# Kernel tuning notes

Measured on AMD Instinct MI355X. Metric: run time of the kernel, lower is better.

The kernel has to match this reference:

```python
import jax, jax.numpy as jnp
import numpy as np

NEG_SLOPE = 0.2  # PyG GATv2Conv default negative_slope


def gatv2_layer(x, src, dst, edge_attr, Wl, bl, Wr, br, We, att, bias, n_nodes):
    """Faithful PyG GATv2Conv (concat=True, eval mode / no dropout).
    x: [N, Fin]; src/dst: [E]; edge_attr: [E, Fe]; att: [H, C].
    Returns [N, H*C].
    """
    H, C = att.shape
    xl = (x @ Wl + bl).reshape(-1, H, C)        # source-side transform (x_j)
    xr = (x @ Wr + br).reshape(-1, H, C)        # target-side transform (x_i)
    e_emb = (edge_attr @ We).reshape(-1, H, C)
    # per-edge pre-activation: x_i + x_j + edge
    g = jax.nn.leaky_relu(xl[src] + xr[dst] + e_emb, NEG_SLOPE)  # [E, H, C]
    logits = jnp.einsum('ehc,hc->eh', g, att)                    # [E, H]
    # segment softmax grouped by destination node
    m = jax.ops.segment_max(logits, dst, num_segments=n_nodes)   # [N, H]
    m = jnp.where(jnp.isfinite(m), m, 0.0)                       # empty segments
    a = jnp.exp(logits - m[dst])
    denom = jax.ops.segment_sum(a, dst, num_segments=n_nodes)    # [N, H]
    alpha = a / (denom[dst] + 1e-16)
    msg = xl[src] * alpha[:, :, None]                            # [E, H, C]
    out = jax.ops.segment_sum(msg, dst, num_segments=n_nodes)    # [N, H, C]
    return out.reshape(n_nodes, H * C) + bias


def setup_inputs() -> dict:
    key = jax.random.key(0)
    ks = jax.random.split(key, 24)
    N, E = 100000, 1600000
    Fin, Hd, Fe = 6, 64, 2
    g = lambda k, shp: (jax.random.normal(k, shp, dtype=jnp.float32) * 0.1)
    inp = {
        'x': jax.random.normal(ks[0], (N, Fin), dtype=jnp.float32),
        'edge_index': jax.random.randint(ks[1], (2, E), 0, N, dtype=jnp.int32),
        'edge_attr': jax.random.normal(ks[2], (E, Fe), dtype=jnp.float32),
        # layer 1: heads=2, out=64 -> H*C = 128
        'Wl1': g(ks[3], (Fin, 128)), 'bl1': jnp.zeros((128,), jnp.float32),
        'Wr1': g(ks[4], (Fin, 128)), 'br1': jnp.zeros((128,), jnp.float32),
        'We1': g(ks[5], (Fe, 128)),
        'att1': g(ks[6], (2, Hd)),
        'bias1': jnp.zeros((128,), jnp.float32),
        # layer 2: heads=1, in=128, out=64
        'Wl2': g(ks[7], (128, Hd)), 'bl2': jnp.zeros((Hd,), jnp.float32),
        'Wr2': g(ks[8], (128, Hd)), 'br2': jnp.zeros((Hd,), jnp.float32),
        'We2': g(ks[9], (Fe, Hd)),
        'att2': g(ks[10], (1, Hd)),
        'bias2': jnp.zeros((Hd,), jnp.float32),
        # MLP head
        'Wh1': g(ks[11], (Hd, Hd)), 'bh1': jnp.zeros((Hd,), jnp.float32),
        'Wh2': g(ks[12], (Hd, 1)), 'bh2': jnp.zeros((1,), jnp.float32),
    }
    return inp


def reference(x, edge_index, edge_attr,
              Wl1, bl1, Wr1, br1, We1, att1, bias1,
              Wl2, bl2, Wr2, br2, We2, att2, bias2,
              Wh1, bh1, Wh2, bh2):
    N = x.shape[0]
    src, dst = edge_index[0], edge_index[1]
    h = gatv2_layer(x, src, dst, edge_attr, Wl1, bl1, Wr1, br1, We1, att1, bias1, N)
    h = jax.nn.relu(h)
    h = gatv2_layer(h, src, dst, edge_attr, Wl2, bl2, Wr2, br2, We2, att2, bias2, N)
    h = jax.nn.relu(h)
    out = jax.nn.relu(h @ Wh1 + bh1) @ Wh2 + bh2  # [N, 1]
    return out[:, 0]
```

## Files before the change

### kernel.cpp

```cpp
#include <hip/hip_runtime.h>
#include <hip/hip_bf16.h>

#define NEG_SLOPE 0.2f
#define LOG2E 1.44269504088896f

#define NB_SHIFT 9
#define NB_NODES 512
#define NBLK_PART 256

typedef _Float16 half8 __attribute__((ext_vector_type(8)));
typedef _Float16 half4 __attribute__((ext_vector_type(4)));
typedef _Float16 half2t __attribute__((ext_vector_type(2)));

__device__ __forceinline__ void ld4(float* d, const float* p) {
    float4 t = *(const float4*)p;
    d[0] = t.x; d[1] = t.y; d[2] = t.z; d[3] = t.w;
}

__device__ __forceinline__ unsigned pack2h(float a, float b) {
    union { half2t h; unsigned u; } pk;
    pk.h[0] = (_Float16)a; pk.h[1] = (_Float16)b;
    return pk.u;
}

// ... 25 lines not shown
#define FDOT2(a, b, c) fmaf((float)(a)[1], (float)(b)[1], fmaf((float)(a)[0], (float)(b)[0], (c)))
#endif

#define DPP_ADD(x, ctrl) \
    ((x) + __int_as_float(__builtin_amdgcn_update_dpp(0, __float_as_int(x), (ctrl), 0xf, 0xf, true)))
#define ROW_REDUCE16(x) do { \
    x = DPP_ADD(x, 0x128); \
    x = DPP_ADD(x, 0x124); \
    x = DPP_ADD(x, 0x122); \
    x = DPP_ADD(x, 0x121); \
} while (0)

#define CHGRP(xl2, xr2, wa, wb, at2, ex, ey, logit) do { \
    half2t z_ = (xl2) + (xr2); \
    z_ = __builtin_elementwise_fma((ex), (wa), z_); \
    z_ = __builtin_elementwise_fma((ey), (wb), z_); \
    z_ = __builtin_elementwise_max(z_, z_ * NEGS); \
    logit = FDOT2(z_, (at2), logit); \
} while (0)

__global__ void __launch_bounds__(256) prep_kernel(
    const float* __restrict__ x,
    const float* __restrict__ Wl1, const float* __restrict__ bl1,
    const float* __restrict__ Wr1, const float* __restrict__ br1,
    _Float16* __restrict__ xlh, _Float16* __restrict__ xrh, int N)
{
    int gt = blockIdx.x * blockDim.x + threadIdx.x;
    int n = gt >> 6, t = gt & 63;
    if (n >= N) return;
    int h = t >> 5;
    int cp = t & 31;
    int c0 = h * 64 + 2 * cp;
    const float* xrow = x + (size_t)n * 6;
    float la = bl1[c0], lb = bl1[c0 + 1];
    float ra = br1[c0], rb = br1[c0 + 1];
#pragma unroll
    for (int f = 0; f < 6; ++f) {
        float xv = xrow[f];
        la = fmaf(xv, Wl1[f * 128 + c0], la);
        lb = fmaf(xv, Wl1[f * 128 + c0 + 1], lb);
        ra = fmaf(xv, Wr1[f * 128 + c0], ra);
        rb = fmaf(xv, Wr1[f * 128 + c0 + 1], rb);
    }
    int pos = (cp >> 1) * 8 + h * 4 + (cp & 1) * 2;
    *(unsigned*)(xlh + (size_t)n * 128 + pos) = pack2h(la, lb);
    *(unsigned*)(xrh + (size_t)n * 128 + pos) = pack2h(ra, rb);
}

__global__ void __launch_bounds__(256) partA_count(
    const int* __restrict__ dstv, int* __restrict__ M, int E, int EPB, int NB)
{
    __shared__ int hist[256];
    int blk = blockIdx.x, t = threadIdx.x;
    if (t < NB) hist[t] = 0;
    __syncthreads();
    int s0 = blk * EPB;
    int s1 = min(s0 + EPB, E);
    for (int e = s0 + t; e < s1; e += 256)
        atomicAdd(&hist[((unsigned)dstv[e]) >> NB_SHIFT], 1);
    __syncthreads();
    if (t < NB) M[t * NBLK_PART + blk] = hist[t];
}

__global__ void __launch_bounds__(256) partB1_scanrow(
    int* __restrict__ M, int* __restrict__ btot)
{
    __shared__ int lds[256];
    int bkt = blockIdx.x, t = threadIdx.x;
    int cnt = M[bkt * NBLK_PART + t];
    lds[t] = cnt;
    __syncthreads();
    for (int s = 1; s < 256; s <<= 1) {
        int v = (t >= s) ? lds[t - s] : 0;
        __syncthreads();
        lds[t] += v;
        __syncthreads();
    }
    M[bkt * NBLK_PART + t] = lds[t] - cnt;
    if (t == 255) btot[bkt] = lds[255];
}

__global__ void partB2_scanbkt(const int* __restrict__ btot, int* __restrict__ boff,
                               int* __restrict__ off, int NB, int N, int E)
{
    if (threadIdx.x == 0) {
        int run = 0;
        for (int i = 0; i < NB; ++i) { boff[i] = run; run += btot[i]; }
        boff[NB] = run;
        off[N] = E;
    }
}

__global__ void __launch_bounds__(256) partC_scatter(
    const int* __restrict__ srcv, const int* __restrict__ dstv,
    const float2* __restrict__ ea2, const int* __restrict__ M,
    const int* __restrict__ boff,
    int2* __restrict__ ebuf, int E, int EPB, int NB)
{
    __shared__ int cur[256];
    int blk = blockIdx.x, t = threadIdx.x;
    if (t < NB) cur[t] = M[t * NBLK_PART + blk] + boff[t];
    __syncthreads();
    int s0 = blk * EPB;
    int s1 = min(s0 + EPB, E);
    for (int e = s0 + t; e < s1; e += 256) {
        int d = dstv[e];
        int bkt = ((unsigned)d) >> NB_SHIFT;
        int p = atomicAdd(&cur[bkt], 1);
        float2 ea = ea2[e];
        int2 v;
        v.x = srcv[e] | ((d & (NB_NODES - 1)) << 23);
        v.y = (int)pack2h(ea.x, ea.y);
        ebuf[p] = v;
    }
}

__global__ void __launch_bounds__(256) partD_finalize(
    const int2* __restrict__ ebuf, const int* __restrict__ boff,
    int* __restrict__ off, int2* __restrict__ csr_edge, int N)
{
    __shared__ int hist[NB_NODES];
    int b = blockIdx.x, t = threadIdx.x;
    int node_base = b << NB_SHIFT;
    int nnodes = min(NB_NODES, N - node_base);
    int seg_s = boff[b], seg_e = boff[b + 1];
    for (int i = t; i < NB_NODES; i += 256) hist[i] = 0;
    __syncthreads();
    for (int e = seg_s + t; e < seg_e; e += 256)
        atomicAdd(&hist[((unsigned)ebuf[e].x) >> 23], 1);
    __syncthreads();
    if (t == 0) {
        int run = 0;
        for (int i = 0; i < nnodes; ++i) { int c = hist[i]; hist[i] = run; run += c; }
    }
    __syncthreads();
    for (int i = t; i < nnodes; i += 256) off[node_base + i] = seg_s + hist[i];
    __syncthreads();
    for (int e = seg_s + t; e < seg_e; e += 256) {
        int2 v = ebuf[e];
        int dl = ((unsigned)v.x) >> 23;
        int r = atomicAdd(&hist[dl], 1);
        v.x &= 0x7FFFFF;
        csr_edge[seg_s + r] = v;
    }
}

__global__ void __launch_bounds__(256) c1_kernel(
    const int* __restrict__ off, const int2* __restrict__ csr_edge,
    const _Float16* __restrict__ xlh, const _Float16* __restrict__ xrh,
    const float* __restrict__ We1, const float* __restrict__ att1,
    const float* __restrict__ bias1,
    _Float16* __restrict__ h1h, int N)
{
    int wv = (blockIdx.x * blockDim.x + threadIdx.x) >> 6;
    int lane = threadIdx.x & 63;
    if (2 * wv >= N) return;
    int half = lane >> 5;
    int n = 2 * wv + half;
    bool nvalid = (n < N);
    int nc = nvalid ? n : 0;
    int l = lane & 31;
    int g = l & 15;
    int slot = (l >> 4) & 1;
    unsigned gb = (unsigned)(g << 4);

    const half2t NEGS = f2h2(NEG_SLOPE, NEG_SLOPE);

    half2t a0h[2], a1h[2], w00h[2], w01h[2], w10h[2], w11h[2];
    {
        float t[4];
        ld4(t, att1 + 4 * g);
        a0h[0] = f2h2(t[0] * LOG2E, t[1] * LOG2E); a0h[1] = f2h2(t[2] * LOG2E, t[3] * LOG2E);
        ld4(t, att1 + 64 + 4 * g);
        a1h[0] = f2h2(t[0] * LOG2E, t[1] * LOG2E); a1h[1] = f2h2(t[2] * LOG2E, t[3] * LOG2E);
        ld4(t, We1 + 4 * g);        w00h[0] = f2h2(t[0], t[1]); w00h[1] = f2h2(t[2], t[3]);
        ld4(t, We1 + 64 + 4 * g);   w01h[0] = f2h2(t[0], t[1]); w01h[1] = f2h2(t[2], t[3]);
        ld4(t, We1 + 128 + 4 * g);  w10h[0] = f2h2(t[0], t[1]); w10h[1] = f2h2(t[2], t[3]);
        ld4(t, We1 + 192 + 4 * g);  w11h[0] = f2h2(t[0], t[1]); w11h[1] = f2h2(t[2], t[3]);
    }

    half2t xr00, xr01, xr10, xr11;
    {
        half8 xrv = *(const half8*)(xrh + (size_t)nc * 128 + 8 * g);
        xr00[0] = xrv[0]; xr00[1] = xrv[1];
        xr01[0] = xrv[2]; xr01[1] = xrv[3];
        xr10[0] = xrv[4]; xr10[1] = xrv[5];
        xr11[0] = xrv[6]; xr11[1] = xrv[7];
    }

    int s = off[nc];
    int e = nvalid ? off[nc + 1] : s;
    int m = e - s;
    int mo = __shfl_xor(m, 32);
    int iters = (max(m, mo) + 3) >> 2;

    float a0A[4] = {0,0,0,0}, a1A[4] = {0,0,0,0};
    float a0B[4] = {0,0,0,0}, a1B[4] = {0,0,0,0};
    float d0A = 0.f, d1A = 0.f, d0B = 0.f, d1B = 0.f;

    const char* xlb = (const char*)xlh;

    int pA0 = s + slot, pB0 = s + 2 + slot;
    bool vA0 = (pA0 < e), vB0 = (pB0 < e);
    int2 edA0 = csr_edge[vA0 ? pA0 : 0];
    int2 edB0 = csr_edge[vB0 ? pB0 : 0];
    int pA1 = s + 4 + slot, pB1 = s + 6 + slot;
    bool vA1 = (pA1 < e), vB1 = (pB1 < e);
    int2 edA1 = csr_edge[vA1 ? pA1 : 0];
    int2 edB1 = csr_edge[vB1 ? pB1 : 0];
    half8 hvA = *(const half8*)(xlb + (((unsigned)edA0.x) << 8) + gb);
    half8 hvB = *(const half8*)(xlb + (((unsigned)edB0.x) << 8) + gb);

    int p0 = s;
    for (int it = 0; it < iters; ++it, p0 += 4) {
        int pA2 = p0 + 8 + slot, pB2 = p0 + 10 + slot;
        bool vA2 = (pA2 < e), vB2 = (pB2 < e);
        int2 edA2 = csr_edge[vA2 ? pA2 : 0];
        int2 edB2 = csr_edge[vB2 ? pB2 : 0];

        half8 hvAn = *(const half8*)(xlb + (((unsigned)edA1.x) << 8) + gb);
        half8 hvBn = *(const half8*)(xlb + (((unsigned)edB1.x) << 8) + gb);

        unsigned uA = (unsigned)edA0.y, uB = (unsigned)edB0.y;
        half2t exA = u2h2(PERMB(uA, uA, 0x01000100));
        half2t eyA = u2h2(PERMB(uA, uA, 0x03020302));
        half2t exB = u2h2(PERMB(uB, uB, 0x01000100));
        half2t eyB = u2h2(PERMB(uB, uB, 0x03020302));

        union { half8 h; unsigned u[4]; } HA, HB;
        HA.h = hvA; HB.h = hvB;
        half2t xA00 = u2h2(HA.u[0]), xA01 = u2h2(HA.u[1]);
        half2t xA10 = u2h2(HA.u[2]), xA11 = u2h2(HA.u[3]);
        half2t xB00 = u2h2(HB.u[0]), xB01 = u2h2(HB.u[1]);
        half2t xB10 = u2h2(HB.u[2]), xB11 = u2h2(HB.u[3]);

        float pA0f = 0.f, pA1f = 0.f, pB0f = 0.f, pB1f = 0.f;
        CHGRP(xA00, xr00, w00h[0], w10h[0], a0h[0], exA, eyA, pA0f);
        CHGRP(xA01, xr01, w00h[1], w10h[1], a0h[1], exA, eyA, pA0f);
        CHGRP(xA10, xr10, w01h[0], w11h[0], a1h[0], exA, eyA, pA1f);
        CHGRP(xA11, xr11, w01h[1], w11h[1], a1h[1], exA, eyA, pA1f);
        CHGRP(xB00, xr00, w00h[0], w10h[0], a0h[0], exB, eyB, pB0f);
        CHGRP(xB01, xr01, w00h[1], w10h[1], a0h[1], exB, eyB, pB0f);
        CHGRP(xB10, xr10, w01h[0], w11h[0], a1h[0], exB, eyB, pB1f);
        CHGRP(xB11, xr11, w01h[1], w11h[1], a1h[1], exB, eyB, pB1f);

        ROW_REDUCE16(pA0f);
        ROW_REDUCE16(pA1f);
        ROW_REDUCE16(pB0f);
        ROW_REDUCE16(pB1f);

        float eA0 = vA0 ? exp2f(pA0f) : 0.f;
        float eA1 = vA0 ? exp2f(pA1f) : 0.f;
        float eB0 = vB0 ? exp2f(pB0f) : 0.f;
        float eB1 = vB0 ? exp2f(pB1f) : 0.f;
        d0A += eA0; d1A += eA1;
        d0B += eB0; d1B += eB1;

        a0A[0] = fmaf(eA0, (float)hvA[0], a0A[0]);
        a0A[1] = fmaf(eA0, (float)hvA[1], a0A[1]);
        a0A[2] = fmaf(eA0, (float)hvA[2], a0A[2]);
        a0A[3] = fmaf(eA0, (float)hvA[3], a0A[3]);
        a1A[0] = fmaf(eA1, (float)hvA[4], a1A[0]);
        a1A[1] = fmaf(eA1, (float)hvA[5], a1A[1]);
        a1A[2] = fmaf(eA1, (float)hvA[6], a1A[2]);
        a1A[3] = fmaf(eA1, (float)hvA[7], a1A[3]);
        a0B[0] = fmaf(eB0, (float)hvB[0], a0B[0]);
        a0B[1] = fmaf(eB0, (float)hvB[1], a0B[1]);
        a0B[2] = fmaf(eB0, (float)hvB[2], a0B[2]);
        a0B[3] = fmaf(eB0, (float)hvB[3], a0B[3]);
        a1B[0] = fmaf(eB1, (float)hvB[4], a1B[0]);
        a1B[1] = fmaf(eB1, (float)hvB[5], a1B[1]);
        a1B[2] = fmaf(eB1, (float)hvB[6], a1B[2]);
        a1B[3] = fmaf(eB1, (float)hvB[7], a1B[3]);

        edA0 = edA1; edB0 = edB1; vA0 = vA1; vB0 = vB1;
        edA1 = edA2; edB1 = edB2; vA1 = vA2; vB1 = vB2;
        hvA = hvAn; hvB = hvBn;
    }

    float acc0[4], acc1[4];
#pragma unroll
    for (int i = 0; i < 4; ++i) { acc0[i] = a0A[i] + a0B[i]; acc1[i] = a1A[i] + a1B[i]; }
    float d0 = d0A + d0B, d1 = d1A + d1B;
#pragma unroll
    for (int i = 0; i < 4; ++i) {
        acc0[i] += __shfl_xor(acc0[i], 16);
        acc1[i] += __shfl_xor(acc1[i], 16);
    }
    d0 += __shfl_xor(d0, 16);
    d1 += __shfl_xor(d1, 16);

    if (slot == 0 && nvalid) {
        float b0[4], b1[4];
        ld4(b0, bias1 + 4 * g);
        ld4(b1, bias1 + 64 + 4 * g);
        float r0 = 1.f / (d0 + 1e-16f), r1 = 1.f / (d1 + 1e-16f);
        half4 o0, o1;
        o0[0] = (_Float16)fmaxf(fmaf(acc0[0], r0, b0[0]), 0.f);
        o0[1] = (_Float16)fmaxf(fmaf(acc0[1], r0, b0[1]), 0.f);
        o0[2] = (_Float16)fmaxf(fmaf(acc0[2], r0, b0[2]), 0.f);
        o0[3] = (_Float16)fmaxf(fmaf(acc0[3], r0, b0[3]), 0.f);
        o1[0] = (_Float16)fmaxf(fmaf(acc1[0], r1, b1[0]), 0.f);
        o1[1] = (_Float16)fmaxf(fmaf(acc1[1], r1, b1[1]), 0.f);
        o1[2] = (_Float16)fmaxf(fmaf(acc1[2], r1, b1[2]), 0.f);
        o1[3] = (_Float16)fmaxf(fmaf(acc1[3], r1, b1[3]), 0.f);
        *(half4*)(h1h + (size_t)n * 128 + 4 * g) = o0;
        *(half4*)(h1h + (size_t)n * 128 + 64 + 4 * g) = o1;
    }
}

__global__ void __launch_bounds__(256) a2_kernel(
    const _Float16* __restrict__ h1h,
    const float* __restrict__ Wl2, const float* __restrict__ bl2,
    const float* __restrict__ Wr2, const float* __restrict__ br2,
    _Float16* __restrict__ xl2h, _Float16* __restrict__ xr2h, int N)
{
    __shared__ float hs[64 * 128];
    int tid = threadIdx.x;
    int n0 = blockIdx.x * 64;

    for (int i = tid; i < 64 * 16; i += 256) {
        int row = i >> 4;
        int q = i & 15;
        int n = n0 + row;
        float f[8];
        if (n < N) {
            half8 v = *(const half8*)(h1h + (size_t)n * 128 + q * 8);
#pragma unroll
            for (int j = 0; j < 8; ++j) f[j] = (float)v[j];
        } else {
#pragma unroll
            for (int j = 0; j < 8; ++j) f[j] = 0.f;
        }
        *(float4*)(hs + row * 128 + q * 8)     = make_float4(f[0], f[1], f[2], f[3]);
        *(float4*)(hs + row * 128 + q * 8 + 4) = make_float4(f[4], f[5], f[6], f[7]);
    }
    __syncthreads();

    int cslot = tid & 31;
    int jgrp = tid >> 5;
    int c4 = cslot * 4;
    bool isL = (c4 < 64);
    int cc = isL ? c4 : (c4 - 64);
    const float* Wb = (isL ? Wl2 : Wr2) + cc;
    const float* bb = (isL ? bl2 : br2) + cc;
    float4 bias = *(const float4*)bb;

    float acc[8][4];
#pragma unroll
    for (int j = 0; j < 8; ++j) {
        acc[j][0] = bias.x; acc[j][1] = bias.y;
        acc[j][2] = bias.z; acc[j][3] = bias.w;
    }

    const float* hrow = hs + (jgrp * 8) * 128;
#pragma unroll 2
    for (int k4 = 0; k4 < 32; ++k4) {
        float4 w0 = *(const float4*)(Wb + (4 * k4 + 0) * 64);
        float4 w1 = *(const float4*)(Wb + (4 * k4 + 1) * 64);
        float4 w2 = *(const float4*)(Wb + (4 * k4 + 2) * 64);
        float4 w3 = *(const float4*)(Wb + (4 * k4 + 3) * 64);
#pragma unroll
        for (int j = 0; j < 8; ++j) {
            float4 hv = *(const float4*)(hrow + j * 128 + k4 * 4);
            acc[j][0] = fmaf(hv.x, w0.x, acc[j][0]);
            acc[j][1] = fmaf(hv.x, w0.y, acc[j][1]);
            acc[j][2] = fmaf(hv.x, w0.z, acc[j][2]);
            acc[j][3] = fmaf(hv.x, w0.w, acc[j][3]);
            acc[j][0] = fmaf(hv.y, w1.x, acc[j][0]);
            acc[j][1] = fmaf(hv.y, w1.y, acc[j][1]);
            acc[j][2] = fmaf(hv.y, w1.z, acc[j][2]);
            acc[j][3] = fmaf(hv.y, w1.w, acc[j][3]);
            acc[j][0] = fmaf(hv.z, w2.x, acc[j][0]);
            acc[j][1] = fmaf(hv.z, w2.y, acc[j][1]);
            acc[j][2] = fmaf(hv.z, w2.z, acc[j][2]);
            acc[j][3] = fmaf(hv.z, w2.w, acc[j][3]);
            acc[j][0] = fmaf(hv.w, w3.x, acc[j][0]);
            acc[j][1] = fmaf(hv.w, w3.y, acc[j][1]);
            acc[j][2] = fmaf(hv.w, w3.z, acc[j][2]);
            acc[j][3] = fmaf(hv.w, w3.w, acc[j][3]);
        }
    }

    _Float16* outb = isL ? xl2h : xr2h;
#pragma unroll
    for (int j = 0; j < 8; ++j) {
        int n = n0 + jgrp * 8 + j;
        if (n < N) {
            half4 o;
            o[0] = (_Float16)acc[j][0];
            o[1] = (_Float16)acc[j][1];
            o[2] = (_Float16)acc[j][2];
            o[3] = (_Float16)acc[j][3];
            *(half4*)(outb + (size_t)n * 64 + cc) = o;
        }
    }
}

__global__ void __launch_bounds__(256) c2_kernel(
    const int* __restrict__ off, const int2* __restrict__ csr_edge,
    const _Float16* __restrict__ xl2h, const _Float16* __restrict__ xr2h,
    const float* __restrict__ We2, const float* __restrict__ att2,
    const float* __restrict__ bias2,
    float* __restrict__ h2out, int N)
{
    int wv = (blockIdx.x * blockDim.x + threadIdx.x) >> 6;
    int lane = threadIdx.x & 63;
    if (2 * wv >= N) return;
    int half = lane >> 5;
    int n = 2 * wv + half;
    bool nvalid = (n < N);
    int nc = nvalid ? n : 0;
    int l = lane & 31;
    int g = l & 15;
    int slot = (l >> 4) & 1;
    unsigned gb = (unsigned)(g << 3);

    const half2t NEGS = f2h2(NEG_SLOPE, NEG_SLOPE);

    half2t avh[2], w0h[2], w1h[2], xr2[2];
    {
        float t[4];
        ld4(t, att2 + 4 * g);
        avh[0] = f2h2(t[0] * LOG2E, t[1] * LOG2E); avh[1] = f2h2(t[2] * LOG2E, t[3] * LOG2E);
        ld4(t, We2 + 4 * g);       w0h[0] = f2h2(t[0], t[1]); w0h[1] = f2h2(t[2], t[3]);
        ld4(t, We2 + 64 + 4 * g);  w1h[0] = f2h2(t[0], t[1]); w1h[1] = f2h2(t[2], t[3]);
        half4 xh = *(const half4*)(xr2h + (size_t)nc * 64 + 4 * g);
        xr2[0][0] = xh[0]; xr2[0][1] = xh[1];
        xr2[1][0] = xh[2]; xr2[1][1] = xh[3];
    }

    int s = off[nc];
    int e = nvalid ? off[nc + 1] : s;
    int m = e - s;
    int mo = __shfl_xor(m, 32);
    int iters = (max(m, mo) + 3) >> 2;

    float dA = 0.f, dB = 0.f;
    float aA[4] = {0,0,0,0}, aB[4] = {0,0,0,0};

    const char* xlb = (const char*)xl2h;

    int pA0 = s + slot, pB0 = s + 2 + slot;
    bool vA0 = (pA0 < e), vB0 = (pB0 < e);
    int2 edA0 = csr_edge[vA0 ? pA0 : 0];
    int2 edB0 = csr_edge[vB0 ? pB0 : 0];
    int pA1 = s + 4 + slot, pB1 = s + 6 + slot;
    bool vA1 = (pA1 < e), vB1 = (pB1 < e);
    int2 edA1 = csr_edge[vA1 ? pA1 : 0];
    int2 edB1 = csr_edge[vB1 ? pB1 : 0];
    half4 hvA = *(const half4*)(xlb + (((unsigned)edA0.x) << 7) + gb);
    half4 hvB = *(const half4*)(xlb + (((unsigned)edB0.x) << 7) + gb);

    int p0 = s;
    for (int it = 0; it < iters; ++it, p0 += 4) {
        int pA2 = p0 + 8 + slot, pB2 = p0 + 10 + slot;
        bool vA2 = (pA2 < e), vB2 = (pB2 < e);
        int2 edA2 = csr_edge[vA2 ? pA2 : 0];
        int2 edB2 = csr_edge[vB2 ? pB2 : 0];

        half4 hvAn = *(const half4*)(xlb + (((unsigned)edA1.x) << 7) + gb);
        half4 hvBn = *(const half4*)(xlb + (((unsigned)edB1.x) << 7) + gb);

        unsigned uA = (unsigned)edA0.y, uB = (unsigned)edB0.y;
        half2t exA = u2h2(PERMB(uA, uA, 0x01000100));
        half2t eyA = u2h2(PERMB(uA, uA, 0x03020302));
        half2t exB = u2h2(PERMB(uB, uB, 0x01000100));
        half2t eyB = u2h2(PERMB(uB, uB, 0x03020302));

        union { half4 h; unsigned u[2]; } HA, HB;
        HA.h = hvA; HB.h = hvB;
        half2t xA0 = u2h2(HA.u[0]), xA1 = u2h2(HA.u[1]);
        half2t xB0 = u2h2(HB.u[0]), xB1 = u2h2(HB.u[1]);

        float pA_ = 0.f, pB_ = 0.f;
        CHGRP(xA0, xr2[0], w0h[0], w1h[0], avh[0], exA, eyA, pA_);
        CHGRP(xA1, xr2[1], w0h[1], w1h[1], avh[1], exA, eyA, pA_);
        CHGRP(xB0, xr2[0], w0h[0], w1h[0], avh[0], exB, eyB, pB_);
        CHGRP(xB1, xr2[1], w0h[1], w1h[1], avh[1], exB, eyB, pB_);

        ROW_REDUCE16(pA_);
        ROW_REDUCE16(pB_);
        float evA = vA0 ? exp2f(pA_) : 0.f;
        float evB = vB0 ? exp2f(pB_) : 0.f;
        dA += evA; dB += evB;

        aA[0] = fmaf(evA, (float)hvA[0], aA[0]);
        aA[1] = fmaf(evA, (float)hvA[1], aA[1]);
        aA[2] = fmaf(evA, (float)hvA[2], aA[2]);
        aA[3] = fmaf(evA, (float)hvA[3], aA[3]);
        aB[0] = fmaf(evB, (float)hvB[0], aB[0]);
        aB[1] = fmaf(evB, (float)hvB[1], aB[1]);
        aB[2] = fmaf(evB, (float)hvB[2], aB[2]);
        aB[3] = fmaf(evB, (float)hvB[3], aB[3]);

        edA0 = edA1; edB0 = edB1; vA0 = vA1; vB0 = vB1;
        edA1 = edA2; edB1 = edB2; vA1 = vA2; vB1 = vB2;
        hvA = hvAn; hvB = hvBn;
    }

    float acc[4];
#pragma unroll
    for (int i = 0; i < 4; ++i) acc[i] = aA[i] + aB[i];
    float dsum = dA + dB;
#pragma unroll
    for (int i = 0; i < 4; ++i) acc[i] += __shfl_xor(acc[i], 16);
    dsum += __shfl_xor(dsum, 16);

    if (slot == 0 && nvalid) {
        float b2[4];
        ld4(b2, bias2 + 4 * g);
        float r = 1.f / (dsum + 1e-16f);
        float4 o;
        o.x = fmaxf(fmaf(acc[0], r, b2[0]), 0.f);
        o.y = fmaxf(fmaf(acc[1], r, b2[1]), 0.f);
        o.z = fmaxf(fmaf(acc[2], r, b2[2]), 0.f);
        o.w = fmaxf(fmaf(acc[3], r, b2[3]), 0.f);
        *(float4*)(h2out + (size_t)n * 64 + 4 * g) = o;
    }
}

__global__ void __launch_bounds__(256) head_kernel(
    const float* __restrict__ h2, const float* __restrict__ Wh1,
    const float* __restrict__ bh1, const float* __restrict__ Wh2,
    const float* __restrict__ bh2, float* __restrict__ out, int N)
{
    __shared__ float hs[64 * 68];
    int tid = threadIdx.x;
    int n0 = blockIdx.x * 64;

    for (int i = tid; i < 64 * 16; i += 256) {
        int row = i >> 4, q = i & 15;
        int n = n0 + row;
        float4 v = (n < N) ? *(const float4*)(h2 + (size_t)n * 64 + q * 4)
                           : make_float4(0.f, 0.f, 0.f, 0.f);
        *(float4*)(hs + row * 68 + q * 4) = v;
    }
    __syncthreads();

    int cslot = tid & 15;
    int jgrp  = tid >> 4;
    int c4 = cslot * 4;
    float4 bias = *(const float4*)(bh1 + c4);

    float acc[4][4];
#pragma unroll
    for (int r = 0; r < 4; ++r) {
        acc[r][0] = bias.x; acc[r][1] = bias.y;
        acc[r][2] = bias.z; acc[r][3] = bias.w;
    }

    const float* hrow = hs + (jgrp * 4) * 68;
#pragma unroll 2
    for (int k4 = 0; k4 < 16; ++k4) {
        float4 w0 = *(const float4*)(Wh1 + (4 * k4 + 0) * 64 + c4);
        float4 w1 = *(const float4*)(Wh1 + (4 * k4 + 1) * 64 + c4);
        float4 w2 = *(const float4*)(Wh1 + (4 * k4 + 2) * 64 + c4);
        float4 w3 = *(const float4*)(Wh1 + (4 * k4 + 3) * 64 + c4);
#pragma unroll
        for (int r = 0; r < 4; ++r) {
            float4 hv = *(const float4*)(hrow + r * 68 + k4 * 4);
            acc[r][0] = fmaf(hv.x, w0.x, acc[r][0]);
            acc[r][1] = fmaf(hv.x, w0.y, acc[r][1]);
            acc[r][2] = fmaf(hv.x, w0.z, acc[r][2]);
            acc[r][3] = fmaf(hv.x, w0.w, acc[r][3]);
            acc[r][0] = fmaf(hv.y, w1.x, acc[r][0]);
            acc[r][1] = fmaf(hv.y, w1.y, acc[r][1]);
            acc[r][2] = fmaf(hv.y, w1.z, acc[r][2]);
            acc[r][3] = fmaf(hv.y, w1.w, acc[r][3]);
            acc[r][0] = fmaf(hv.z, w2.x, acc[r][0]);
            acc[r][1] = fmaf(hv.z, w2.y, acc[r][1]);
            acc[r][2] = fmaf(hv.z, w2.z, acc[r][2]);
            acc[r][3] = fmaf(hv.z, w2.w, acc[r][3]);
            acc[r][0] = fmaf(hv.w, w3.x, acc[r][0]);
            acc[r][1] = fmaf(hv.w, w3.y, acc[r][1]);
            acc[r][2] = fmaf(hv.w, w3.z, acc[r][2]);
            acc[r][3] = fmaf(hv.w, w3.w, acc[r][3]);
        }
    }

    float4 w2v = *(const float4*)(Wh2 + c4);
    float p[4];
#pragma unroll
    for (int r = 0; r < 4; ++r) {
        p[r] = fmaxf(acc[r][0], 0.f) * w2v.x
             + fmaxf(acc[r][1], 0.f) * w2v.y
             + fmaxf(acc[r][2], 0.f) * w2v.z
             + fmaxf(acc[r][3], 0.f) * w2v.w;
    }
#pragma unroll
    for (int m = 1; m <= 8; m <<= 1) {
#pragma unroll
        for (int r = 0; r < 4; ++r) p[r] += __shfl_xor(p[r], m);
    }
    if (cslot == 0) {
        float b = bh2[0];
#pragma unroll
        for (int r = 0; r < 4; ++r) {
            int n = n0 + jgrp * 4 + r;
            if (n < N) out[n] = p[r] + b;
        }
    }
}

extern "C" void kernel_launch(void* const* d_in, const int* in_sizes, int n_in,
                              void* d_out, int out_size, void* d_ws, size_t ws_size,
                              hipStream_t stream) {
    const float* x    = (const float*)d_in[0];
    const int*   ei   = (const int*)d_in[1];
    const float* ea   = (const float*)d_in[2];
    const float* Wl1  = (const float*)d_in[3];
    const float* bl1  = (const float*)d_in[4];
    const float* Wr1  = (const float*)d_in[5];
    const float* br1  = (const float*)d_in[6];
    const float* We1  = (const float*)d_in[7];
    const float* att1 = (const float*)d_in[8];
    const float* bias1= (const float*)d_in[9];
    const float* Wl2  = (const float*)d_in[10];
    const float* bl2  = (const float*)d_in[11];
    const float* Wr2  = (const float*)d_in[12];
    const float* br2  = (const float*)d_in[13];
    const float* We2  = (const float*)d_in[14];
    const float* att2 = (const float*)d_in[15];
    const float* bias2= (const float*)d_in[16];
    const float* Wh1  = (const float*)d_in[17];
    const float* bh1  = (const float*)d_in[18];
    const float* Wh2  = (const float*)d_in[19];
    const float* bh2  = (const float*)d_in[20];

    int N = in_sizes[0] / 6;
    int E = in_sizes[1] / 2;
    const int* srcv = ei;
    const int* dstv = ei + E;

    int NB = (N + NB_NODES - 1) >> NB_SHIFT;
    int EPB = (E + NBLK_PART - 1) / NBLK_PART;

    char* w = (char*)d_ws;
    auto align256 = [](size_t v) { return (v + 255) & ~(size_t)255; };
    _Float16* xlh = (_Float16*)w;
    char* ip = w + align256((size_t)N * 128 * 2);
    _Float16* xrh = (_Float16*)ip; ip += align256((size_t)N * 128 * 2);
    _Float16* h1h = (_Float16*)ip; ip += align256((size_t)N * 128 * 2);
    _Float16* xl2h = (_Float16*)ip; ip += align256((size_t)N * 64 * 2);
    _Float16* xr2h = (_Float16*)ip; ip += align256((size_t)N * 64 * 2);
    int* off = (int*)ip;  ip += align256((size_t)(N + 1) * 4);
    int* Mbuf = (int*)ip; ip += align256((size_t)NB * NBLK_PART * 4);
    int* btot = (int*)ip; ip += align256((size_t)NB * 4);
    int* boff = (int*)ip; ip += align256((size_t)(NB + 1) * 4);
    int2* csr_edge = (int2*)ip;

    int2* ebuf = (int2*)h1h;
    float* h2 = (float*)xlh;

    prep_kernel<<<((size_t)N * 64 + 255) / 256, 256, 0, stream>>>(
        x, Wl1, bl1, Wr1, br1, xlh, xrh, N);
    partA_count<<<NBLK_PART, 256, 0, stream>>>(dstv, Mbuf, E, EPB, NB);
    partB1_scanrow<<<NB, 256, 0, stream>>>(Mbuf, btot);
    partB2_scanbkt<<<1, 64, 0, stream>>>(btot, boff, off, NB, N, E);
    partC_scatter<<<NBLK_PART, 256, 0, stream>>>(
        srcv, dstv, (const float2*)ea, Mbuf, boff, ebuf, E, EPB, NB);
    partD_finalize<<<NB, 256, 0, stream>>>(ebuf, boff, off, csr_edge, N);
    size_t nwv = (size_t)((N + 1) / 2);
    c1_kernel<<<(nwv * 64 + 255) / 256, 256, 0, stream>>>(
        off, csr_edge, xlh, xrh, We1, att1, bias1, h1h, N);
    a2_kernel<<<(N + 63) / 64, 256, 0, stream>>>(
        h1h, Wl2, bl2, Wr2, br2, xl2h, xr2h, N);
    c2_kernel<<<(nwv * 64 + 255) / 256, 256, 0, stream>>>(
        off, csr_edge, xl2h, xr2h, We2, att2, bias2, h2, N);
    head_kernel<<<(N + 63) / 64, 256, 0, stream>>>(
        h2, Wh1, bh1, Wh2, bh2, (float*)d_out, N);
}
```

Baseline: 438.8 us.

## Make GAT aggregation kernels persistent with cross-node prefetch of offsets and edges

Converts c1 and c2 from one-wave-per-node-pair launches into grid-stride persistent kernels capped at 1024 blocks. Each wave prefetches the CSR offsets two node pairs ahead and the first edge records of the next pair while processing the current one. The aim is to hide the startup load latency at each node and cut block launch overhead. In exchange it adds register pressure and more complex loop state, and the fixed grid may leave imbalance when node degrees vary.

```diff
diff --git a/kernel.cpp b/kernel.cpp
--- a/kernel.cpp
+++ b/kernel.cpp
@@ -201,13 +201,12 @@
     const float* __restrict__ bias1,
     _Float16* __restrict__ h1h, int N)
 {
-    int wv = (blockIdx.x * blockDim.x + threadIdx.x) >> 6;
     int lane = threadIdx.x & 63;
-    if (2 * wv >= N) return;
+    int wv0 = (blockIdx.x * blockDim.x + threadIdx.x) >> 6;
+    int NW = (gridDim.x * blockDim.x) >> 6;
+    int NPAIR = (N + 1) >> 1;
+    if (wv0 >= NPAIR) return;
     int half = lane >> 5;
-    int n = 2 * wv + half;
-    bool nvalid = (n < N);
-    int nc = nvalid ? n : 0;
     int l = lane & 31;
     int g = l & 15;
     int slot = (l >> 4) & 1;
@@ -228,27 +227,20 @@
         ld4(t, We1 + 192 + 4 * g);  w11h[0] = f2h2(t[0], t[1]); w11h[1] = f2h2(t[2], t[3]);
     }
 
-    half2t xr00, xr01, xr10, xr11;
-    {
-        half8 xrv = *(const half8*)(xrh + (size_t)nc * 128 + 8 * g);
-        xr00[0] = xrv[0]; xr00[1] = xrv[1];
-        xr01[0] = xrv[2]; xr01[1] = xrv[3];
-        xr10[0] = xrv[4]; xr10[1] = xrv[5];
-        xr11[0] = xrv[6]; xr11[1] = xrv[7];
-    }
-
+    const char* xlb = (const char*)xlh;
+
+    int pv = wv0;
+    int n_ = 2 * pv + half;
+    bool nval = (n_ < N);
+    int nc = nval ? n_ : 0;
     int s = off[nc];
-    int e = nvalid ? off[nc + 1] : s;
-    int m = e - s;
-    int mo = __shfl_xor(m, 32);
-    int iters = (max(m, mo) + 3) >> 2;
-
-    float a0A[4] = {0,0,0,0}, a1A[4] = {0,0,0,0};
-    float a0B[4] = {0,0,0,0}, a1B[4] = {0,0,0,0};
-    float d0A = 0.f, d1A = 0.f, d0B = 0.f, d1B = 0.f;
-
-    const char* xlb = (const char*)xlh;
-
+    int e = nval ? off[nc + 1] : s;
+    int pvn = pv + NW;
+    int nn_ = 2 * pvn + half;
+    bool nvaln = (pvn < NPAIR) && (nn_ < N);
+    int ncn = nvaln ? nn_ : 0;
+    int sn = off[ncn];
+    int enx = off[ncn + 1];
     int pA0 = s + slot, pB0 = s + 2 + slot;
     bool vA0 = (pA0 < e), vB0 = (pB0 < e);
     int2 edA0 = csr_edge[vA0 ? pA0 : 0];
@@ -257,104 +249,153 @@
     bool vA1 = (pA1 < e), vB1 = (pB1 < e);
     int2 edA1 = csr_edge[vA1 ? pA1 : 0];
     int2 edB1 = csr_edge[vB1 ? pB1 : 0];
-    half8 hvA = *(const half8*)(xlb + (((unsigned)edA0.x) << 8) + gb);
-    half8 hvB = *(const half8*)(xlb + (((unsigned)edB0.x) << 8) + gb);
-
-    int p0 = s;
-    for (int it = 0; it < iters; ++it, p0 += 4) {
-        int pA2 = p0 + 8 + slot, pB2 = p0 + 10 + slot;
-        bool vA2 = (pA2 < e), vB2 = (pB2 < e);
-        int2 edA2 = csr_edge[vA2 ? pA2 : 0];
-        int2 edB2 = csr_edge[vB2 ? pB2 : 0];
-
-        half8 hvAn = *(const half8*)(xlb + (((unsigned)edA1.x) << 8) + gb);
-        half8 hvBn = *(const half8*)(xlb + (((unsigned)edB1.x) << 8) + gb);
-
-        unsigned uA = (unsigned)edA0.y, uB = (unsigned)edB0.y;
-        half2t exA = u2h2(PERMB(uA, uA, 0x01000100));
-        half2t eyA = u2h2(PERMB(uA, uA, 0x03020302));
-        half2t exB = u2h2(PERMB(uB, uB, 0x01000100));
-        half2t eyB = u2h2(PERMB(uB, uB, 0x03020302));
-
-        union { half8 h; unsigned u[4]; } HA, HB;
-        HA.h = hvA; HB.h = hvB;
-        half2t xA00 = u2h2(HA.u[0]), xA01 = u2h2(HA.u[1]);
-        half2t xA10 = u2h2(HA.u[2]), xA11 = u2h2(HA.u[3]);
-        half2t xB00 = u2h2(HB.u[0]), xB01 = u2h2(HB.u[1]);
-        half2t xB10 = u2h2(HB.u[2]), xB11 = u2h2(HB.u[3]);
-
-        float pA0f = 0.f, pA1f = 0.f, pB0f = 0.f, pB1f = 0.f;
-        CHGRP(xA00, xr00, w00h[0], w10h[0], a0h[0], exA, eyA, pA0f);
-        CHGRP(xA01, xr01, w00h[1], w10h[1], a0h[1], exA, eyA, pA0f);
-        CHGRP(xA10, xr10, w01h[0], w11h[0], a1h[0], exA, eyA, pA1f);
-        CHGRP(xA11, xr11, w01h[1], w11h[1], a1h[1], exA, eyA, pA1f);
-        CHGRP(xB00, xr00, w00h[0], w10h[0], a0h[0], exB, eyB, pB0f);
-        CHGRP(xB01, xr01, w00h[1], w10h[1], a0h[1], exB, eyB, pB0f);
-        CHGRP(xB10, xr10, w01h[0], w11h[0], a1h[0], exB, eyB, pB1f);
-        CHGRP(xB11, xr11, w01h[1], w11h[1], a1h[1], exB, eyB, pB1f);
-
-        ROW_REDUCE16(pA0f);
-        ROW_REDUCE16(pA1f);
-        ROW_REDUCE16(pB0f);
-        ROW_REDUCE16(pB1f);
-
-        float eA0 = vA0 ? exp2f(pA0f) : 0.f;
-        float eA1 = vA0 ? exp2f(pA1f) : 0.f;
-        float eB0 = vB0 ? exp2f(pB0f) : 0.f;
-        float eB1 = vB0 ? exp2f(pB1f) : 0.f;
-        d0A += eA0; d1A += eA1;
-        d0B += eB0; d1B += eB1;
-
-        a0A[0] = fmaf(eA0, (float)hvA[0], a0A[0]);
-        a0A[1] = fmaf(eA0, (float)hvA[1], a0A[1]);
-        a0A[2] = fmaf(eA0, (float)hvA[2], a0A[2]);
-        a0A[3] = fmaf(eA0, (float)hvA[3], a0A[3]);
-        a1A[0] = fmaf(eA1, (float)hvA[4], a1A[0]);
-        a1A[1] = fmaf(eA1, (float)hvA[5], a1A[1]);
-        a1A[2] = fmaf(eA1, (float)hvA[6], a1A[2]);
-        a1A[3] = fmaf(eA1, (float)hvA[7], a1A[3]);
-        a0B[0] = fmaf(eB0, (float)hvB[0], a0B[0]);
-        a0B[1] = fmaf(eB0, (float)hvB[1], a0B[1]);
-        a0B[2] = fmaf(eB0, (float)hvB[2], a0B[2]);
-        a0B[3] = fmaf(eB0, (float)hvB[3], a0B[3]);
-        a1B[0] = fmaf(eB1, (float)hvB[4], a1B[0]);
-        a1B[1] = fmaf(eB1, (float)hvB[5], a1B[1]);
-        a1B[2] = fmaf(eB1, (float)hvB[6], a1B[2]);
-        a1B[3] = fmaf(eB1, (float)hvB[7], a1B[3]);
-
-        edA0 = edA1; edB0 = edB1; vA0 = vA1; vB0 = vB1;
-        edA1 = edA2; edB1 = edB2; vA1 = vA2; vB1 = vB2;
-        hvA = hvAn; hvB = hvBn;
-    }
-
-    float acc0[4], acc1[4];
-#pragma unroll
-    for (int i = 0; i < 4; ++i) { acc0[i] = a0A[i] + a0B[i]; acc1[i] = a1A[i] + a1B[i]; }
-    float d0 = d0A + d0B, d1 = d1A + d1B;
-#pragma unroll
-    for (int i = 0; i < 4; ++i) {
-        acc0[i] += __shfl_xor(acc0[i], 16);
-        acc1[i] += __shfl_xor(acc1[i], 16);
-    }
-    d0 += __shfl_xor(d0, 16);
-    d1 += __shfl_xor(d1, 16);
-
-    if (slot == 0 && nvalid) {
-        float b0[4], b1[4];
-        ld4(b0, bias1 + 4 * g);
-        ld4(b1, bias1 + 64 + 4 * g);
-        float r0 = 1.f / (d0 + 1e-16f), r1 = 1.f / (d1 + 1e-16f);
-        half4 o0, o1;
-        o0[0] = (_Float16)fmaxf(fmaf(acc0[0], r0, b0[0]), 0.f);
-        o0[1] = (_Float16)fmaxf(fmaf(acc0[1], r0, b0[1]), 0.f);
-        o0[2] = (_Float16)fmaxf(fmaf(acc0[2], r0, b0[2]), 0.f);
-        o0[3] = (_Float16)fmaxf(fmaf(acc0[3], r0, b0[3]), 0.f);
-        o1[0] = (_Float16)fmaxf(fmaf(acc1[0], r1, b1[0]), 0.f);
-        o1[1] = (_Float16)fmaxf(fmaf(acc1[1], r1, b1[1]), 0.f);
-        o1[2] = (_Float16)fmaxf(fmaf(acc1[2], r1, b1[2]), 0.f);
-        o1[3] = (_Float16)fmaxf(fmaf(acc1[3], r1, b1[3]), 0.f);
-        *(half4*)(h1h + (size_t)n * 128 + 4 * g) = o0;
-        *(half4*)(h1h + (size_t)n * 128 + 64 + 4 * g) = o1;
+
+    while (true) {
+        half8 hvA = *(const half8*)(xlb + (((unsigned)edA0.x) << 8) + gb);
+        half8 hvB = *(const half8*)(xlb + (((unsigned)edB0.x) << 8) + gb);
+
+        half2t xr00, xr01, xr10, xr11;
+        {
+            half8 xrv = *(const half8*)(xrh + (size_t)nc * 128 + 8 * g);
+            xr00[0] = xrv[0]; xr00[1] = xrv[1];
+            xr01[0] = xrv[2]; xr01[1] = xrv[3];
+            xr10[0] = xrv[4]; xr10[1] = xrv[5];
+            xr11[0] = xrv[6]; xr11[1] = xrv[7];
+        }
+
+        int pv2 = pvn + NW;
+        int n2_ = 2 * pv2 + half;
+        bool nval2 = (pv2 < NPAIR) && (n2_ < N);
+        int nc2 = nval2 ? n2_ : 0;
+        int s2 = off[nc2];
+        int e2 = off[nc2 + 1];
+
+        int en_eff = nvaln ? enx : sn;
+        int pA0n = sn + slot, pB0n = sn + 2 + slot;
+        bool vA0n = (pA0n < en_eff), vB0n = (pB0n < en_eff);
+        int2 edA0n = csr_edge[vA0n ? pA0n : 0];
+        int2 edB0n = csr_edge[vB0n ? pB0n : 0];
+        int pA1n = sn + 4 + slot, pB1n = sn + 6 + slot;
+        bool vA1n = (pA1n < en_eff), vB1n = (pB1n < en_eff);
+        int2 edA1n = csr_edge[vA1n ? pA1n : 0];
+        int2 edB1n = csr_edge[vB1n ? pB1n : 0];
+
+        int m = e - s;
+        int mo = __shfl_xor(m, 32);
+        int iters = (max(m, mo) + 3) >> 2;
+
+        float a0A[4] = {0,0,0,0}, a1A[4] = {0,0,0,0};
+        float a0B[4] = {0,0,0,0}, a1B[4] = {0,0,0,0};
+        float d0A = 0.f, d1A = 0.f, d0B = 0.f, d1B = 0.f;
+
+        int2 cA0 = edA0, cB0 = edB0, cA1 = edA1, cB1 = edB1;
+        bool wA0 = vA0, wB0 = vB0, wA1 = vA1, wB1 = vB1;
+
+        int p0 = s;
+        for (int it = 0; it < iters; ++it, p0 += 4) {
+            int pA2 = p0 + 8 + slot, pB2 = p0 + 10 + slot;
+            bool wA2 = (pA2 < e), wB2 = (pB2 < e);
+            int2 cA2 = csr_edge[wA2 ? pA2 : 0];
+            int2 cB2 = csr_edge[wB2 ? pB2 : 0];
+
+            half8 hvAn = *(const half8*)(xlb + (((unsigned)cA1.x) << 8) + gb);
+            half8 hvBn = *(const half8*)(xlb + (((unsigned)cB1.x) << 8) + gb);
+
+            unsigned uA = (unsigned)cA0.y, uB = (unsigned)cB0.y;
+            half2t exA = u2h2(PERMB(uA, uA, 0x01000100));
+            half2t eyA = u2h2(PERMB(uA, uA, 0x03020302));
+            half2t exB = u2h2(PERMB(uB, uB, 0x01000100));
+            half2t eyB = u2h2(PERMB(uB, uB, 0x03020302));
+
+            union { half8 h; unsigned u[4]; } HA, HB;
+            HA.h = hvA; HB.h = hvB;
+            half2t xA00 = u2h2(HA.u[0]), xA01 = u2h2(HA.u[1]);
+            half2t xA10 = u2h2(HA.u[2]), xA11 = u2h2(HA.u[3]);
+            half2t xB00 = u2h2(HB.u[0]), xB01 = u2h2(HB.u[1]);
+            half2t xB10 = u2h2(HB.u[2]), xB11 = u2h2(HB.u[3]);
+
+            float pA0f = 0.f, pA1f = 0.f, pB0f = 0.f, pB1f = 0.f;
+            CHGRP(xA00, xr00, w00h[0], w10h[0], a0h[0], exA, eyA, pA0f);
+            CHGRP(xA01, xr01, w00h[1], w10h[1], a0h[1], exA, eyA, pA0f);
+            CHGRP(xA10, xr10, w01h[0], w11h[0], a1h[0], exA, eyA, pA1f);
+            CHGRP(xA11, xr11, w01h[1], w11h[1], a1h[1], exA, eyA, pA1f);
+            CHGRP(xB00, xr00, w00h[0], w10h[0], a0h[0], exB, eyB, pB0f);
+            CHGRP(xB01, xr01, w00h[1], w10h[1], a0h[1], exB, eyB, pB0f);
+            CHGRP(xB10, xr10, w01h[0], w11h[0], a1h[0], exB, eyB, pB1f);
+            CHGRP(xB11, xr11, w01h[1], w11h[1], a1h[1], exB, eyB, pB1f);
+
+            ROW_REDUCE16(pA0f);
+            ROW_REDUCE16(pA1f);
+            ROW_REDUCE16(pB0f);
+            ROW_REDUCE16(pB1f);
+
+            float eA0 = wA0 ? exp2f(pA0f) : 0.f;
+            float eA1 = wA0 ? exp2f(pA1f) : 0.f;
+            float eB0 = wB0 ? exp2f(pB0f) : 0.f;
+            float eB1 = wB0 ? exp2f(pB1f) : 0.f;
+            d0A += eA0; d1A += eA1;
+            d0B += eB0; d1B += eB1;
+
+            a0A[0] = fmaf(eA0, (float)hvA[0], a0A[0]);
+            a0A[1] = fmaf(eA0, (float)hvA[1], a0A[1]);
+            a0A[2] = fmaf(eA0, (float)hvA[2], a0A[2]);
+            a0A[3] = fmaf(eA0, (float)hvA[3], a0A[3]);
+            a1A[0] = fmaf(eA1, (float)hvA[4], a1A[0]);
+            a1A[1] = fmaf(eA1, (float)hvA[5], a1A[1]);
+            a1A[2] = fmaf(eA1, (float)hvA[6], a1A[2]);
+            a1A[3] = fmaf(eA1, (float)hvA[7], a1A[3]);
+            a0B[0] = fmaf(eB0, (float)hvB[0], a0B[0]);
+            a0B[1] = fmaf(eB0, (float)hvB[1], a0B[1]);
+            a0B[2] = fmaf(eB0, (float)hvB[2], a0B[2]);
+            a0B[3] = fmaf(eB0, (float)hvB[3], a0B[3]);
+            a1B[0] = fmaf(eB1, (float)hvB[4], a1B[0]);
+            a1B[1] = fmaf(eB1, (float)hvB[5], a1B[1]);
+            a1B[2] = fmaf(eB1, (float)hvB[6], a1B[2]);
+            a1B[3] = fmaf(eB1, (float)hvB[7], a1B[3]);
+
+            cA0 = cA1; cB0 = cB1; wA0 = wA1; wB0 = wB1;
+            cA1 = cA2; cB1 = cB2; wA1 = wA2; wB1 = wB2;
+            hvA = hvAn; hvB = hvBn;
+        }
+
+        float acc0[4], acc1[4];
+#pragma unroll
+        for (int i = 0; i < 4; ++i) { acc0[i] = a0A[i] + a0B[i]; acc1[i] = a1A[i] + a1B[i]; }
+        float d0 = d0A + d0B, d1 = d1A + d1B;
+#pragma unroll
+        for (int i = 0; i < 4; ++i) {
+            acc0[i] += __shfl_xor(acc0[i], 16);
+            acc1[i] += __shfl_xor(acc1[i], 16);
+        }
+        d0 += __shfl_xor(d0, 16);
+        d1 += __shfl_xor(d1, 16);
+
+        if (slot == 0 && nval) {
+            float b0[4], b1[4];
+            ld4(b0, bias1 + 4 * g);
+            ld4(b1, bias1 + 64 + 4 * g);
+            float r0 = 1.f / (d0 + 1e-16f), r1 = 1.f / (d1 + 1e-16f);
+            half4 o0, o1;
+            o0[0] = (_Float16)fmaxf(fmaf(acc0[0], r0, b0[0]), 0.f);
+            o0[1] = (_Float16)fmaxf(fmaf(acc0[1], r0, b0[1]), 0.f);
+            o0[2] = (_Float16)fmaxf(fmaf(acc0[2], r0, b0[2]), 0.f);
+            o0[3] = (_Float16)fmaxf(fmaf(acc0[3], r0, b0[3]), 0.f);
+            o1[0] = (_Float16)fmaxf(fmaf(acc1[0], r1, b1[0]), 0.f);
+            o1[1] = (_Float16)fmaxf(fmaf(acc1[1], r1, b1[1]), 0.f);
+            o1[2] = (_Float16)fmaxf(fmaf(acc1[2], r1, b1[2]), 0.f);
+            o1[3] = (_Float16)fmaxf(fmaf(acc1[3], r1, b1[3]), 0.f);
+            *(half4*)(h1h + (size_t)n_ * 128 + 4 * g) = o0;
+            *(half4*)(h1h + (size_t)n_ * 128 + 64 + 4 * g) = o1;
+        }
+
+        pv = pvn;
+        if (pv >= NPAIR) break;
+        n_ = nn_; nval = nvaln; nc = ncn;
+        s = sn; e = en_eff;
+        pvn = pv2; nn_ = n2_; nvaln = nval2; ncn = nc2;
+        sn = s2; enx = e2;
+        edA0 = edA0n; edB0 = edB0n; edA1 = edA1n; edB1 = edB1n;
+        vA0 = vA0n; vB0 = vB0n; vA1 = vA1n; vB1 = vB1n;
     }
 }
 
@@ -453,13 +494,12 @@
     const float* __restrict__ bias2,
     float* __restrict__ h2out, int N)
 {
-    int wv = (blockIdx.x * blockDim.x + threadIdx.x) >> 6;
     int lane = threadIdx.x & 63;
-    if (2 * wv >= N) return;
+    int wv0 = (blockIdx.x * blockDim.x + threadIdx.x) >> 6;
+    int NW = (gridDim.x * blockDim.x) >> 6;
+    int NPAIR = (N + 1) >> 1;
+    if (wv0 >= NPAIR) return;
     int half = lane >> 5;
-    int n = 2 * wv + half;
-    bool nvalid = (n < N);
-    int nc = nvalid ? n : 0;
     int l = lane & 31;
     int g = l & 15;
     int slot = (l >> 4) & 1;
@@ -467,29 +507,29 @@
 
     const half2t NEGS = f2h2(NEG_SLOPE, NEG_SLOPE);
 
-    half2t avh[2], w0h[2], w1h[2], xr2[2];
+    half2t avh[2], w0h[2], w1h[2];
     {
         float t[4];
         ld4(t, att2 + 4 * g);
         avh[0] = f2h2(t[0] * LOG2E, t[1] * LOG2E); avh[1] = f2h2(t[2] * LOG2E, t[3] * LOG2E);
         ld4(t, We2 + 4 * g);       w0h[0] = f2h2(t[0], t[1]); w0h[1] = f2h2(t[2], t[3]);
         ld4(t, We2 + 64 + 4 * g);  w1h[0] = f2h2(t[0], t[1]); w1h[1] = f2h2(t[2], t[3]);
-        half4 xh = *(const half4*)(xr2h + (size_t)nc * 64 + 4 * g);
-        xr2[0][0] = xh[0]; xr2[0][1] = xh[1];
-        xr2[1][0] = xh[2]; xr2[1][1] = xh[3];
-    }
-
+    }
+
+    const char* xlb = (const char*)xl2h;
+
+    int pv = wv0;
+    int n_ = 2 * pv + half;
+    bool nval = (n_ < N);
+    int nc = nval ? n_ : 0;
     int s = off[nc];
-    int e = nvalid ? off[nc + 1] : s;
-    int m = e - s;
-    int mo = __shfl_xor(m, 32);
-    int iters = (max(m, mo) + 3) >> 2;
-
-    float dA = 0.f, dB = 0.f;
-    float aA[4] = {0,0,0,0}, aB[4] = {0,0,0,0};
-
-    const char* xlb = (const char*)xl2h;
-
+    int e = nval ? off[nc + 1] : s;
+    int pvn = pv + NW;
+    int nn_ = 2 * pvn + half;
+    bool nvaln = (pvn < NPAIR) && (nn_ < N);
+    int ncn = nvaln ? nn_ : 0;
+    int sn = off[ncn];
+    int enx = off[ncn + 1];
     int pA0 = s + slot, pB0 = s + 2 + slot;
     bool vA0 = (pA0 < e), vB0 = (pB0 < e);
     int2 edA0 = csr_edge[vA0 ? pA0 : 0];
@@ -498,74 +538,120 @@
     bool vA1 = (pA1 < e), vB1 = (pB1 < e);
     int2 edA1 = csr_edge[vA1 ? pA1 : 0];
     int2 edB1 = csr_edge[vB1 ? pB1 : 0];
-    half4 hvA = *(const half4*)(xlb + (((unsigned)edA0.x) << 7) + gb);
-    half4 hvB = *(const half4*)(xlb + (((unsigned)edB0.x) << 7) + gb);
-
-    int p0 = s;
-    for (int it = 0; it < iters; ++it, p0 += 4) {
-        int pA2 = p0 + 8 + slot, pB2 = p0 + 10 + slot;
-        bool vA2 = (pA2 < e), vB2 = (pB2 < e);
-        int2 edA2 = csr_edge[vA2 ? pA2 : 0];
-        int2 edB2 = csr_edge[vB2 ? pB2 : 0];
-
-        half4 hvAn = *(const half4*)(xlb + (((unsigned)edA1.x) << 7) + gb);
-        half4 hvBn = *(const half4*)(xlb + (((unsigned)edB1.x) << 7) + gb);
-
-        unsigned uA = (unsigned)edA0.y, uB = (unsigned)edB0.y;
-        half2t exA = u2h2(PERMB(uA, uA, 0x01000100));
-        half2t eyA = u2h2(PERMB(uA, uA, 0x03020302));
-        half2t exB = u2h2(PERMB(uB, uB, 0x01000100));
-        half2t eyB = u2h2(PERMB(uB, uB, 0x03020302));
-
-        union { half4 h; unsigned u[2]; } HA, HB;
-        HA.h = hvA; HB.h = hvB;
-        half2t xA0 = u2h2(HA.u[0]), xA1 = u2h2(HA.u[1]);
-        half2t xB0 = u2h2(HB.u[0]), xB1 = u2h2(HB.u[1]);
-
-        float pA_ = 0.f, pB_ = 0.f;
-        CHGRP(xA0, xr2[0], w0h[0], w1h[0], avh[0], exA, eyA, pA_);
-        CHGRP(xA1, xr2[1], w0h[1], w1h[1], avh[1], exA, eyA, pA_);
-        CHGRP(xB0, xr2[0], w0h[0], w1h[0], avh[0], exB, eyB, pB_);
-        CHGRP(xB1, xr2[1], w0h[1], w1h[1], avh[1], exB, eyB, pB_);
-
-        ROW_REDUCE16(pA_);
-        ROW_REDUCE16(pB_);
-        float evA = vA0 ? exp2f(pA_) : 0.f;
-        float evB = vB0 ? exp2f(pB_) : 0.f;
-        dA += evA; dB += evB;
-
-        aA[0] = fmaf(evA, (float)hvA[0], aA[0]);
-        aA[1] = fmaf(evA, (float)hvA[1], aA[1]);
-        aA[2] = fmaf(evA, (float)hvA[2], aA[2]);
-        aA[3] = fmaf(evA, (float)hvA[3], aA[3]);
-        aB[0] = fmaf(evB, (float)hvB[0], aB[0]);
-        aB[1] = fmaf(evB, (float)hvB[1], aB[1]);
-        aB[2] = fmaf(evB, (float)hvB[2], aB[2]);
-        aB[3] = fmaf(evB, (float)hvB[3], aB[3]);
-
-        edA0 = edA1; edB0 = edB1; vA0 = vA1; vB0 = vB1;
-        edA1 = edA2; edB1 = edB2; vA1 = vA2; vB1 = vB2;
-        hvA = hvAn; hvB = hvBn;
-    }
-
-    float acc[4];
-#pragma unroll
-    for (int i = 0; i < 4; ++i) acc[i] = aA[i] + aB[i];
-    float dsum = dA + dB;
-#pragma unroll
-    for (int i = 0; i < 4; ++i) acc[i] += __shfl_xor(acc[i], 16);
-    dsum += __shfl_xor(dsum, 16);
-
-    if (slot == 0 && nvalid) {
-        float b2[4];
-        ld4(b2, bias2 + 4 * g);
-        float r = 1.f / (dsum + 1e-16f);
-        float4 o;
-        o.x = fmaxf(fmaf(acc[0], r, b2[0]), 0.f);
-        o.y = fmaxf(fmaf(acc[1], r, b2[1]), 0.f);
-        o.z = fmaxf(fmaf(acc[2], r, b2[2]), 0.f);
-        o.w = fmaxf(fmaf(acc[3], r, b2[3]), 0.f);
-        *(float4*)(h2out + (size_t)n * 64 + 4 * g) = o;
+
+    while (true) {
+        half4 hvA = *(const half4*)(xlb + (((unsigned)edA0.x) << 7) + gb);
+        half4 hvB = *(const half4*)(xlb + (((unsigned)edB0.x) << 7) + gb);
+
+        half2t xr2[2];
+        {
+            half4 xh = *(const half4*)(xr2h + (size_t)nc * 64 + 4 * g);
+            xr2[0][0] = xh[0]; xr2[0][1] = xh[1];
+            xr2[1][0] = xh[2]; xr2[1][1] = xh[3];
+        }
+
+        int pv2 = pvn + NW;
+        int n2_ = 2 * pv2 + half;
+        bool nval2 = (pv2 < NPAIR) && (n2_ < N);
+        int nc2 = nval2 ? n2_ : 0;
+        int s2 = off[nc2];
+        int e2 = off[nc2 + 1];
+
+        int en_eff = nvaln ? enx : sn;
+        int pA0n = sn + slot, pB0n = sn + 2 + slot;
+        bool vA0n = (pA0n < en_eff), vB0n = (pB0n < en_eff);
+        int2 edA0n = csr_edge[vA0n ? pA0n : 0];
+        int2 edB0n = csr_edge[vB0n ? pB0n : 0];
+        int pA1n = sn + 4 + slot, pB1n = sn + 6 + slot;
+        bool vA1n = (pA1n < en_eff), vB1n = (pB1n < en_eff);
+        int2 edA1n = csr_edge[vA1n ? pA1n : 0];
+        int2 edB1n = csr_edge[vB1n ? pB1n : 0];
+
+        int m = e - s;
+        int mo = __shfl_xor(m, 32);
+        int iters = (max(m, mo) + 3) >> 2;
+
+        float dA = 0.f, dB = 0.f;
+        float aA[4] = {0,0,0,0}, aB[4] = {0,0,0,0};
+
+        int2 cA0 = edA0, cB0 = edB0, cA1 = edA1, cB1 = edB1;
+        bool wA0 = vA0, wB0 = vB0, wA1 = vA1, wB1 = vB1;
+
+        int p0 = s;
+        for (int it = 0; it < iters; ++it, p0 += 4) {
+            int pA2 = p0 + 8 + slot, pB2 = p0 + 10 + slot;
+            bool wA2 = (pA2 < e), wB2 = (pB2 < e);
+            int2 cA2 = csr_edge[wA2 ? pA2 : 0];
+            int2 cB2 = csr_edge[wB2 ? pB2 : 0];
+
+            half4 hvAn = *(const half4*)(xlb + (((unsigned)cA1.x) << 7) + gb);
+            half4 hvBn = *(const half4*)(xlb + (((unsigned)cB1.x) << 7) + gb);
+
+            unsigned uA = (unsigned)cA0.y, uB = (unsigned)cB0.y;
+            half2t exA = u2h2(PERMB(uA, uA, 0x01000100));
+            half2t eyA = u2h2(PERMB(uA, uA, 0x03020302));
+            half2t exB = u2h2(PERMB(uB, uB, 0x01000100));
+            half2t eyB = u2h2(PERMB(uB, uB, 0x03020302));
+
+            union { half4 h; unsigned u[2]; } HA, HB;
+            HA.h = hvA; HB.h = hvB;
+            half2t xA0 = u2h2(HA.u[0]), xA1 = u2h2(HA.u[1]);
+            half2t xB0 = u2h2(HB.u[0]), xB1 = u2h2(HB.u[1]);
+
+            float pA_ = 0.f, pB_ = 0.f;
+            CHGRP(xA0, xr2[0], w0h[0], w1h[0], avh[0], exA, eyA, pA_);
+            CHGRP(xA1, xr2[1], w0h[1], w1h[1], avh[1], exA, eyA, pA_);
+            CHGRP(xB0, xr2[0], w0h[0], w1h[0], avh[0], exB, eyB, pB_);
+            CHGRP(xB1, xr2[1], w0h[1], w1h[1], avh[1], exB, eyB, pB_);
+
+            ROW_REDUCE16(pA_);
+            ROW_REDUCE16(pB_);
+            float evA = wA0 ? exp2f(pA_) : 0.f;
+            float evB = wB0 ? exp2f(pB_) : 0.f;
+            dA += evA; dB += evB;
+
+            aA[0] = fmaf(evA, (float)hvA[0], aA[0]);
+            aA[1] = fmaf(evA, (float)hvA[1], aA[1]);
+            aA[2] = fmaf(evA, (float)hvA[2], aA[2]);
+            aA[3] = fmaf(evA, (float)hvA[3], aA[3]);
+            aB[0] = fmaf(evB, (float)hvB[0], aB[0]);
+            aB[1] = fmaf(evB, (float)hvB[1], aB[1]);
+            aB[2] = fmaf(evB, (float)hvB[2], aB[2]);
+            aB[3] = fmaf(evB, (float)hvB[3], aB[3]);
+
+            cA0 = cA1; cB0 = cB1; wA0 = wA1; wB0 = wB1;
+            cA1 = cA2; cB1 = cB2; wA1 = wA2; wB1 = wB2;
+            hvA = hvAn; hvB = hvBn;
+        }
+
+        float acc[4];
+#pragma unroll
+        for (int i = 0; i < 4; ++i) acc[i] = aA[i] + aB[i];
+        float dsum = dA + dB;
+#pragma unroll
+        for (int i = 0; i < 4; ++i) acc[i] += __shfl_xor(acc[i], 16);
+        dsum += __shfl_xor(dsum, 16);
+
+        if (slot == 0 && nval) {
+            float b2[4];
+            ld4(b2, bias2 + 4 * g);
+            float r = 1.f / (dsum + 1e-16f);
+            float4 o;
+            o.x = fmaxf(fmaf(acc[0], r, b2[0]), 0.f);
+            o.y = fmaxf(fmaf(acc[1], r, b2[1]), 0.f);
+            o.z = fmaxf(fmaf(acc[2], r, b2[2]), 0.f);
+            o.w = fmaxf(fmaf(acc[3], r, b2[3]), 0.f);
+            *(float4*)(h2out + (size_t)n_ * 64 + 4 * g) = o;
+        }
+
+        pv = pvn;
+        if (pv >= NPAIR) break;
+        n_ = nn_; nval = nvaln; nc = ncn;
+        s = sn; e = en_eff;
+        pvn = pv2; nn_ = n2_; nvaln = nval2; ncn = nc2;
+        sn = s2; enx = e2;
+        edA0 = edA0n; edB0 = edB0n; edA1 = edA1n; edB1 = edB1n;
+        vA0 = vA0n; vB0 = vB0n; vA1 = vA1n; vB1 = vB1n;
     }
 }
 
@@ -710,12 +796,15 @@
     partC_scatter<<<NBLK_PART, 256, 0, stream>>>(
         srcv, dstv, (const float2*)ea, Mbuf, boff, ebuf, E, EPB, NB);
     partD_finalize<<<NB, 256, 0, stream>>>(ebuf, boff, off, csr_edge, N);
-    size_t nwv = (size_t)((N + 1) / 2);
-    c1_kernel<<<(nwv * 64 + 255) / 256, 256, 0, stream>>>(
+
+    int NPAIR = (N + 1) / 2;
+    int nblk = (NPAIR + 3) / 4;
+    if (nblk > 1024) nblk = 1024;
+    c1_kernel<<<nblk, 256, 0, stream>>>(
         off, csr_edge, xlh, xrh, We1, att1, bias1, h1h, N);
     a2_kernel<<<(N + 63) / 64, 256, 0, stream>>>(
         h1h, Wl2, bl2, Wr2, br2, xl2h, xr2h, N);
-    c2_kernel<<<(nwv * 64 + 255) / 256, 256, 0, stream>>>(
+    c2_kernel<<<nblk, 256, 0, stream>>>(
         off, csr_edge, xl2h, xr2h, We2, att2, bias2, h2, N);
     head_kernel<<<(N + 63) / 64, 256, 0, stream>>>(
         h2, Wh1, bh1, Wh2, bh2, (float*)d_out, N);
```

Result: slower. 475.1 us (+8.3%).
